# Kernel tuning notes

Hardware: AMD Instinct MI355X
Metric: run time of the kernel (lower is better)

## Reference

```python
import jax, jax.numpy as jnp
import numpy as np

B, D, W, KVAL = 8192, 768, 8192, 32  # batch, input_dim, width, mp_kval


def setup_inputs() -> dict:
    key = jax.random.key(0)
    k1, k2 = jax.random.split(key)
    x = jax.random.normal(k1, (B, D), dtype=jnp.float32)
    # decoder dictionary Ad: [input_dim, width], kaiming-ish scale
    Ad = jax.random.normal(k2, (D, W), dtype=jnp.float32) / np.float32(np.sqrt(D))
    bd = jnp.zeros((1, D), dtype=jnp.float32)
    return {"x": x, "Ad": Ad, "bd": bd}


def reference(x, Ad, bd):
    # Matching-pursuit branch of SAE.forward (sae_type == 'MP')
    Ad_n = Ad / jnp.clip(jnp.linalg.norm(Ad, axis=0, keepdims=True), 1e-8)  # [D, W]
    resid0 = x - bd                                    # [B, D]
    codes0 = jnp.zeros((x.shape[0], Ad.shape[1]), x.dtype)  # [B, W]
    sel0 = jnp.zeros_like(codes0)                      # [B, W]
    rows = jnp.arange(x.shape[0])

    def step(carry, _):
        resid, codes, sel = carry
        z = resid @ Ad_n                               # [B, W] projection
        z = jnp.where(sel > 0, 0.0, z)                 # mask already-selected atoms
        idx = jnp.argmax(jnp.abs(z), axis=1)           # [B] greedy top-1
        val = jnp.take_along_axis(z, idx[:, None], axis=1)  # [B, 1]
        codes = codes.at[rows, idx].add(val[:, 0])
        sel = sel.at[rows, idx].add(1.0)
        # rank-1 residual update: (one_hot(idx)*val) @ Ad_n.T == val * Ad_n[:, idx].T
        resid = resid - val * jnp.take(Ad_n.T, idx, axis=0)  # [B, D]
        return (resid, codes, sel), None

    (resid, codes, sel), _ = jax.lax.scan(step, (resid0, codes0, sel0), None, length=KVAL)
    return codes @ Ad_n.T + bd
```

## Files before the change

### kernel.cpp

```cpp
#include <hip/hip_runtime.h>
#include <cstddef>

static const int WW = 8192;
static const int DD = 768;
static const int BBATCH = 8192;
static const int KSEL = 32;

typedef double f64x4 __attribute__((ext_vector_type(4)));

__device__ inline void mfma_f64_probe(int lane, int* pi, int* pj) {
    f64x4 z0{0.0, 0.0, 0.0, 0.0};
    f64x4 d1 = __builtin_amdgcn_mfma_f64_16x16x4f64((double)lane, 1.0, z0, 0, 0, 0);
    f64x4 d2 = __builtin_amdgcn_mfma_f64_16x16x4f64(1.0, (double)lane, z0, 0, 0, 0);
#pragma unroll
    for (int v = 0; v < 4; ++v) {
        pi[v] = (((int)d1[v] - 96) >> 2) & 15;
        pj[v] = (((int)d2[v] - 96) >> 2) & 15;
    }
}

__global__ __launch_bounds__(256) void colnorm_kernel(const float* __restrict__ Ad,
                                                      float* __restrict__ nrm) {
    int w = blockIdx.x * 256 + threadIdx.x;
    double s = 0.0;
    for (int d = 0; d < DD; ++d) {
        double v = (double)Ad[(size_t)d * WW + w];
        s += v * v;
    }
    nrm[w] = fmaxf((float)sqrt(s), 1e-8f);
}

__global__ __launch_bounds__(256) void transpose_scale_kernel(const float* __restrict__ Ad,
                                                              const float* __restrict__ nrm,
                                                              float* __restrict__ AdnT) {
    __shared__ float tile[32][33];
    int wb = blockIdx.x * 32;
    int db = blockIdx.y * 32;
    int tx = threadIdx.x;
    int ty = threadIdx.y;
    for (int i = ty; i < 32; i += 8)
        tile[i][tx] = Ad[(size_t)(db + i) * WW + (wb + tx)];
    __syncthreads();
    for (int i = ty; i < 32; i += 8)
        AdnT[(size_t)(wb + i) * DD + (db + tx)] = tile[tx][i] / nrm[wb + i];
}

__global__ __launch_bounds__(256, 2) void gram_mfma_f64_kernel(const float* __restrict__ Ad,
                                                               const float* __restrict__ nrm,
                                                               float* __restrict__ G) {
    const int bx = blockIdx.x, by = blockIdx.y;
    if (bx < 2 * by) return;
    __shared__ __align__(16) double As[32 * 130];
    __shared__ __align__(16) double Bs[32 * 66];
    const int tid = threadIdx.x;
    const int lane = tid & 63;
    const int wv = tid >> 6;
    const int wr = wv >> 1;
    const int wc = wv & 1;
    const int i0 = by * 128;
    const int j0 = bx * 64;
    const int ar0 = tid >> 6;
    const int ap0 = (tid & 63) * 2;
    const int brow = tid >> 5;
    const int bpos = (tid & 31) * 2;

    f64x4 acc[4][2];
#pragma unroll
    for (int m = 0; m < 4; ++m)
#pragma unroll
        for (int n = 0; n < 2; ++n)
            acc[m][n] = f64x4{0.0, 0.0, 0.0, 0.0};

    float2 aL[8], bl[4];
#pragma unroll
    for (int q = 0; q < 8; ++q)
        aL[q] = *(const float2*)&Ad[(size_t)(4 * q + ar0) * WW + i0 + ap0];
#pragma unroll
    for (int s = 0; s < 4; ++s)
        bl[s] = *(const float2*)&Ad[(size_t)(8 * s + brow) * WW + j0 + bpos];

    for (int k0 = 0; k0 < DD; k0 += 32) {
        __syncthreads();
#pragma unroll
        for (int q = 0; q < 8; ++q) {
            double2 da; da.x = (double)aL[q].x; da.y = (double)aL[q].y;
            *(double2*)&As[(4 * q + ar0) * 130 + ap0] = da;
        }
#pragma unroll
        for (int s = 0; s < 4; ++s) {
            double2 d0; d0.x = (double)bl[s].x; d0.y = (double)bl[s].y;
            *(double2*)&Bs[(8 * s + brow) * 66 + bpos] = d0;
        }
        __syncthreads();
        if (k0 + 32 < DD) {
#pragma unroll
            for (int q = 0; q < 8; ++q)
                aL[q] = *(const float2*)&Ad[(size_t)(k0 + 32 + 4 * q + ar0) * WW + i0 + ap0];
#pragma unroll
            for (int s = 0; s < 4; ++s)
                bl[s] = *(const float2*)&Ad[(size_t)(k0 + 32 + 8 * s + brow) * WW + j0 + bpos];
        }
#pragma unroll
        for (int kc = 0; kc < 8; ++kc) {
            const int krow = kc * 4 + (lane >> 4);
            const double* ap = &As[krow * 130 + wr * 64 + (lane & 15)];
            const double* bp = &Bs[krow * 66 + wc * 32 + (lane & 15)];
            double aF[4], bF[2];
#pragma unroll
            for (int m = 0; m < 4; ++m) aF[m] = ap[m * 16];
#pragma unroll
            for (int n = 0; n < 2; ++n) bF[n] = bp[n * 16];
#pragma unroll
            for (int m = 0; m < 4; ++m)
#pragma unroll
                for (int n = 0; n < 2; ++n)
                    acc[m][n] = __builtin_amdgcn_mfma_f64_16x16x4f64(aF[m], bF[n],
                                                                     acc[m][n], 0, 0, 0);
        }
    }

    int pi[4], pj[4];
    mfma_f64_probe(lane, pi, pj);
#pragma unroll
    for (int m = 0; m < 4; ++m) {
#pragma unroll
        for (int v = 0; v < 4; ++v) {
            int row = i0 + wr * 64 + m * 16 + pi[v];
            double inv_i = 1.0 / (double)nrm[row];
#pragma unroll
            for (int n = 0; n < 2; ++n) {
                int col = j0 + wc * 32 + n * 16 + pj[v];
                G[(size_t)row * WW + col] = (float)(acc[m][n][v] * inv_i / (double)nrm[col]);
            }
        }
    }
}

__global__ __launch_bounds__(256) void mirror_kernel(float* __restrict__ G) {
    const int ti = blockIdx.y;
    const int tj = blockIdx.x;
    if (tj <= ti) return;
    __shared__ float tile[64][65];
    const int t = threadIdx.x;
    const int c4 = (t & 15) * 4;
    const int r  = t >> 4;
#pragma unroll
    for (int rr = r; rr < 64; rr += 16) {
        float4 v = *(const float4*)&G[(size_t)(ti * 64 + rr) * WW + tj * 64 + c4];
        tile[rr][c4 + 0] = v.x;
        tile[rr][c4 + 1] = v.y;
        tile[rr][c4 + 2] = v.z;
        tile[rr][c4 + 3] = v.w;
    }
    __syncthreads();
#pragma unroll
    for (int rr = r; rr < 64; rr += 16) {
        float4 v = make_float4(tile[c4 + 0][rr], tile[c4 + 1][rr],
                               tile[c4 + 2][rr], tile[c4 + 3][rr]);
        *(float4*)&G[(size_t)(tj * 64 + rr) * WW + ti * 64 + c4] = v;
    }
}

__global__ __launch_bounds__(256, 2) void z_mfma_f64_kernel(const float* __restrict__ X,
                                                            const float* __restrict__ Ad,
                                                            const float* __restrict__ bd,
                                                            const float* __restrict__ nrm,
                                                            float* __restrict__ Z) {
    __shared__ __align__(16) double As[32 * 66];
    __shared__ __align__(16) double Bs[32 * 130];
    const int tid = threadIdx.x;
    const int lane = tid & 63;
    const int wc = tid >> 6;
    const int b0 = blockIdx.y * 64;
    const int w0 = blockIdx.x * 128;
    const int r  = tid >> 2;
    const int k8 = (tid & 3) * 8;
    const int br0 = tid >> 6;
    const int bp0 = (tid & 63) * 2;

    f64x4 acc[4][2];
#pragma unroll
    for (int m = 0; m < 4; ++m)
#pragma unroll
        for (int n = 0; n < 2; ++n)
            acc[m][n] = f64x4{0.0, 0.0, 0.0, 0.0};

    float4 a0L, a1L; float2 bL[8];
    {
        float4 bias0 = *(const float4*)&bd[k8];
        float4 bias1 = *(const float4*)&bd[k8 + 4];
        float4 a0 = *(const float4*)&X[(size_t)(b0 + r) * DD + k8];
        float4 a1 = *(const float4*)&X[(size_t)(b0 + r) * DD + k8 + 4];
        a0.x -= bias0.x; a0.y -= bias0.y; a0.z -= bias0.z; a0.w -= bias0.w;
        a1.x -= bias1.x; a1.y -= bias1.y; a1.z -= bias1.z; a1.w -= bias1.w;
        a0L = a0; a1L = a1;
#pragma unroll
        for (int q = 0; q < 8; ++q)
            bL[q] = *(const float2*)&Ad[(size_t)(4 * q + br0) * WW + w0 + bp0];
    }

    for (int k0 = 0; k0 < DD; k0 += 32) {
        __syncthreads();
        As[(k8 + 0) * 66 + r] = (double)a0L.x;
        As[(k8 + 1) * 66 + r] = (double)a0L.y;
        As[(k8 + 2) * 66 + r] = (double)a0L.z;
        As[(k8 + 3) * 66 + r] = (double)a0L.w;
        As[(k8 + 4) * 66 + r] = (double)a1L.x;
        As[(k8 + 5) * 66 + r] = (double)a1L.y;
        As[(k8 + 6) * 66 + r] = (double)a1L.z;
        As[(k8 + 7) * 66 + r] = (double)a1L.w;
#pragma unroll
        for (int q = 0; q < 8; ++q) {
            double2 db; db.x = (double)bL[q].x; db.y = (double)bL[q].y;
            *(double2*)&Bs[(4 * q + br0) * 130 + bp0] = db;
        }
        __syncthreads();
        if (k0 + 32 < DD) {
            const int kn = k0 + 32;
            float4 bias0 = *(const float4*)&bd[kn + k8];
            float4 bias1 = *(const float4*)&bd[kn + k8 + 4];
            float4 a0 = *(const float4*)&X[(size_t)(b0 + r) * DD + kn + k8];
            float4 a1 = *(const float4*)&X[(size_t)(b0 + r) * DD + kn + k8 + 4];
            a0.x -= bias0.x; a0.y -= bias0.y; a0.z -= bias0.z; a0.w -= bias0.w;
            a1.x -= bias1.x; a1.y -= bias1.y; a1.z -= bias1.z; a1.w -= bias1.w;
            a0L = a0; a1L = a1;
#pragma unroll
            for (int q = 0; q < 8; ++q)
                bL[q] = *(const float2*)&Ad[(size_t)(kn + 4 * q + br0) * WW + w0 + bp0];
        }
#pragma unroll
        for (int kc = 0; kc < 8; ++kc) {
            const int krow = kc * 4 + (lane >> 4);
            const double* ap = &As[krow * 66 + (lane & 15)];
            const double* bp = &Bs[krow * 130 + wc * 32 + (lane & 15)];
            double aF[4], bF[2];
#pragma unroll
            for (int m = 0; m < 4; ++m) aF[m] = ap[m * 16];
#pragma unroll
            for (int n = 0; n < 2; ++n) bF[n] = bp[n * 16];
#pragma unroll
            for (int m = 0; m < 4; ++m)
#pragma unroll
                for (int n = 0; n < 2; ++n)
                    acc[m][n] = __builtin_amdgcn_mfma_f64_16x16x4f64(aF[m], bF[n],
                                                                     acc[m][n], 0, 0, 0);
        }
    }

    int pi[4], pj[4];
    mfma_f64_probe(lane, pi, pj);
#pragma unroll
    for (int m = 0; m < 4; ++m) {
#pragma unroll
        for (int v = 0; v < 4; ++v) {
            int row = b0 + m * 16 + pi[v];
#pragma unroll
            for (int n = 0; n < 2; ++n) {
                int col = w0 + wc * 32 + n * 16 + pj[v];
                Z[(size_t)row * WW + col] = (float)(acc[m][n][v] / (double)nrm[col]);
            }
        }
    }
}

__global__ __launch_bounds__(256) void mp_loop_kernel(const float* __restrict__ z0,
                                                      const float* __restrict__ G,
                                                      int* __restrict__ idxL,
                                                      float* __restrict__ valL) {
    __shared__ __align__(16) float zrow[WW];
    __shared__ float wv[4];
    __shared__ int   wi[4];
    const int b = blockIdx.x;
    const int t = threadIdx.x;
    float4* zs = (float4*)zrow;

    float best = -1.f;
    int bidx = 0;
    unsigned selmask = 0;

    {
        const float4* zp = (const float4*)(z0 + (size_t)b * WW);
#pragma unroll
        for (int j = 0; j < 8; ++j) {
            int slot = t + 256 * j;
            float4 v = zp[slot];
            zs[slot] = v;
            int w = slot * 4;
            float a0 = fabsf(v.x), a1 = fabsf(v.y), a2 = fabsf(v.z), a3 = fabsf(v.w);
            if (a0 > best) { best = a0; bidx = w; }
            if (a1 > best) { best = a1; bidx = w + 1; }
            if (a2 > best) { best = a2; bidx = w + 2; }
            if (a3 > best) { best = a3; bidx = w + 3; }
        }
    }

    for (int k = 0; k < KSEL; ++k) {
        float v = best;
        int i = bidx;
#pragma unroll
        for (int off = 32; off > 0; off >>= 1) {
            float ov = __shfl_xor(v, off, 64);
            int   oi = __shfl_xor(i, off, 64);
            if (ov > v || (ov == v && oi < i)) { v = ov; i = oi; }
        }
        if ((t & 63) == 0) { wv[t >> 6] = v; wi[t >> 6] = i; }
        __syncthreads();
        float rv = wv[0];
        int   ri = wi[0];
#pragma unroll
        for (int q = 1; q < 4; ++q) {
            float qv = wv[q];
            int   qi = wi[q];
            if (qv > rv || (qv == rv && qi < ri)) { rv = qv; ri = qi; }
        }
        const int idx = ri;
        const float val = zrow[idx];
        if (t == 0) {
            idxL[(size_t)b * KSEL + k] = idx;
            valL[(size_t)b * KSEL + k] = val;
        }
        if (((idx >> 2) & 255) == t)
            selmask |= 1u << (((idx >> 10) << 2) | (idx & 3));
        if (k == KSEL - 1) break;
        __syncthreads();

        best = -1.f;
        bidx = 0;
        const float4* gr = (const float4*)(G + (size_t)idx * WW);
#pragma unroll
        for (int j = 0; j < 8; ++j) {
            int slot = t + 256 * j;
            float4 g = gr[slot];
            float4 z = zs[slot];
            unsigned m = (selmask >> (j * 4)) & 0xFu;
            float n0 = (m & 1u) ? 0.f : z.x - val * g.x;
            float n1 = (m & 2u) ? 0.f : z.y - val * g.y;
            float n2 = (m & 4u) ? 0.f : z.z - val * g.z;
            float n3 = (m & 8u) ? 0.f : z.w - val * g.w;
            zs[slot] = make_float4(n0, n1, n2, n3);
            int w = slot * 4;
            float a0 = fabsf(n0), a1 = fabsf(n1), a2 = fabsf(n2), a3 = fabsf(n3);
            if (a0 > best) { best = a0; bidx = w; }
            if (a1 > best) { best = a1; bidx = w + 1; }
            if (a2 > best) { best = a2; bidx = w + 2; }
            if (a3 > best) { best = a3; bidx = w + 3; }
        }
    }
}

__global__ __launch_bounds__(256) void copy_meta_kernel(const int* __restrict__ si,
                                                        const float* __restrict__ sv,
                                                        int* __restrict__ di,
                                                        float* __restrict__ dv,
                                                        int n) {
    int i = blockIdx.x * 256 + threadIdx.x;
    if (i < n) {
        di[i] = si[i];
        dv[i] = sv[i];
    }
}

__global__ __launch_bounds__(256) void assemble_kernel(const float* __restrict__ AdnT,
                                                       const float* __restrict__ bd,
                                                       const int* __restrict__ idxL,
                                                       const float* __restrict__ valL,
                                                       float* __restrict__ out,
                                                       int rowStart) {
    __shared__ int sidx[KSEL];
    __shared__ float sval[KSEL];
    const int b = blockIdx.x;
    const int row = rowStart + b;
    const int t = threadIdx.x;
    if (t < KSEL) {
        sidx[t] = idxL[(size_t)b * KSEL + t];
        sval[t] = valL[(size_t)b * KSEL + t];
    }
    __syncthreads();
    float acc0 = bd[t];
    float acc1 = bd[t + 256];
    float acc2 = bd[t + 512];
#pragma unroll 4
    for (int k = 0; k < KSEL; ++k) {
        const float* col = AdnT + (size_t)sidx[k] * DD;
        float v = sval[k];
        acc0 += v * col[t];
        acc1 += v * col[t + 256];
        acc2 += v * col[t + 512];
    }
    out[(size_t)row * DD + t] = acc0;
    out[(size_t)row * DD + t + 256] = acc1;
    out[(size_t)row * DD + t + 512] = acc2;
}

extern "C" void kernel_launch(void* const* d_in, const int* in_sizes, int n_in,
                              void* d_out, int out_size, void* d_ws, size_t ws_size,
                              hipStream_t stream) {
    const float* x  = (const float*)d_in[0];
    const float* Ad = (const float*)d_in[1];
    const float* bd = (const float*)d_in[2];
    float* out = (float*)d_out;

    const size_t ADNT_B = (size_t)WW * DD * 4;
    const size_t NRM_B  = (size_t)WW * 4;
    const size_t IDX_B  = (size_t)BBATCH * KSEL * 4;
    const size_t VAL_B  = IDX_B;
    const size_t G_B    = (size_t)WW * WW * 4;
    const size_t ZROW_B = (size_t)WW * 4;
    const size_t A_MIN  = ADNT_B + NRM_B + IDX_B + VAL_B + G_B + 128 * ZROW_B;

    if (ws_size >= A_MIN) {
        char* p = (char*)d_ws;
        float* AdnT = (float*)p;  p += ADNT_B;
        float* nrm  = (float*)p;  p += NRM_B;
        int*   idxL = (int*)p;    p += IDX_B;
        float* valL = (float*)p;  p += VAL_B;
        float* G    = (float*)p;  p += G_B;
        float* z    = (float*)p;
        size_t z_avail = ws_size - (ADNT_B + NRM_B + IDX_B + VAL_B + G_B);
        int chunk = (int)((z_avail / ZROW_B) / 128) * 128;
        if (chunk > BBATCH) chunk = BBATCH;

        colnorm_kernel<<<WW / 256, 256, 0, stream>>>(Ad, nrm);
        gram_mfma_f64_kernel<<<dim3(WW / 64, WW / 128), 256, 0, stream>>>(Ad, nrm, G);
        mirror_kernel<<<dim3(WW / 64, WW / 64), 256, 0, stream>>>(G);
        for (int r0 = 0; r0 < BBATCH; r0 += chunk) {
            int rows = (BBATCH - r0 < chunk) ? (BBATCH - r0) : chunk;
            z_mfma_f64_kernel<<<dim3(WW / 128, rows / 64), 256, 0, stream>>>(
                x + (size_t)r0 * DD, Ad, bd, nrm, z);
            mp_loop_kernel<<<rows, 256, 0, stream>>>(
                z, G, idxL + (size_t)r0 * KSEL, valL + (size_t)r0 * KSEL);
        }
        transpose_scale_kernel<<<dim3(WW / 32, DD / 32), dim3(32, 8), 0, stream>>>(Ad, nrm, AdnT);
        assemble_kernel<<<BBATCH, 256, 0, stream>>>(AdnT, bd, idxL, valL, out, 0);
    } else if (ws_size >= G_B) {
        float* G    = (float*)d_ws;
        char*  ob   = (char*)d_out;
        float* z    = (float*)ob;
        float* nrm  = (float*)(ob + 20971520);
        int*   idxL = (int*)(ob + 23068672);
        float* valL = (float*)(ob + 24117248);
        float* AdnT = (float*)d_ws;
        int*   idx2 = (int*)((char*)d_ws + ADNT_B);
        float* val2 = (float*)((char*)d_ws + ADNT_B + IDX_B);
        const int chunk = 512;

        colnorm_kernel<<<WW / 256, 256, 0, stream>>>(Ad, nrm);
        gram_mfma_f64_kernel<<<dim3(WW / 64, WW / 128), 256, 0, stream>>>(Ad, nrm, G);
        mirror_kernel<<<dim3(WW / 64, WW / 64), 256, 0, stream>>>(G);
        for (int r0 = 0; r0 < BBATCH; r0 += chunk) {
            int rows = (BBATCH - r0 < chunk) ? (BBATCH - r0) : chunk;
            z_mfma_f64_kernel<<<dim3(WW / 128, rows / 64), 256, 0, stream>>>(
                x + (size_t)r0 * DD, Ad, bd, nrm, z);
            mp_loop_kernel<<<rows, 256, 0, stream>>>(
                z, G, idxL + (size_t)r0 * KSEL, valL + (size_t)r0 * KSEL);
        }
        {
            int n = BBATCH * KSEL;
            copy_meta_kernel<<<(n + 255) / 256, 256, 0, stream>>>(idxL, valL, idx2, val2, n);
        }
        transpose_scale_kernel<<<dim3(WW / 32, DD / 32), dim3(32, 8), 0, stream>>>(Ad, nrm, AdnT);
        assemble_kernel<<<BBATCH, 256, 0, stream>>>(AdnT, bd, idx2, val2, out, 0);
    }
}
```

Baseline: 4.459 ms.

## Fuse z-projection and MP loop into one pipelined kernel with double-buffered chunks

Replaces the alternating z_mfma and mp_loop launches with one fused kernel per step. In each launch, some blocks run the matching-pursuit loop on chunk i-1 while other blocks compute the z projection for chunk i into the other half of a double buffer, so the compute-bound GEMM overlaps the latency-bound MP loop. Chunk size drops to 256 rows. Separately, the Gram kernel's K-tile shrinks from 32 to 16 to cut shared memory per block. The cost is more launches and heterogeneous blocks sharing a 49KB shared-memory footprint, which may limit occupancy.

```diff
diff --git a/kernel.cpp b/kernel.cpp
--- a/kernel.cpp
+++ b/kernel.cpp
@@ -50,8 +50,8 @@
                                                                float* __restrict__ G) {
     const int bx = blockIdx.x, by = blockIdx.y;
     if (bx < 2 * by) return;
-    __shared__ __align__(16) double As[32 * 130];
-    __shared__ __align__(16) double Bs[32 * 66];
+    __shared__ __align__(16) double As[16 * 130];
+    __shared__ __align__(16) double Bs[16 * 66];
     const int tid = threadIdx.x;
     const int lane = tid & 63;
     const int wv = tid >> 6;
@@ -71,37 +71,36 @@
         for (int n = 0; n < 2; ++n)
             acc[m][n] = f64x4{0.0, 0.0, 0.0, 0.0};
 
-    float2 aL[8], bl[4];
-#pragma unroll
-    for (int q = 0; q < 8; ++q)
+    float2 aL[4], bl0, bl1;
+#pragma unroll
+    for (int q = 0; q < 4; ++q)
         aL[q] = *(const float2*)&Ad[(size_t)(4 * q + ar0) * WW + i0 + ap0];
-#pragma unroll
-    for (int s = 0; s < 4; ++s)
-        bl[s] = *(const float2*)&Ad[(size_t)(8 * s + brow) * WW + j0 + bpos];
-
-    for (int k0 = 0; k0 < DD; k0 += 32) {
-        __syncthreads();
-#pragma unroll
-        for (int q = 0; q < 8; ++q) {
+    bl0 = *(const float2*)&Ad[(size_t)(brow) * WW + j0 + bpos];
+    bl1 = *(const float2*)&Ad[(size_t)(8 + brow) * WW + j0 + bpos];
+
+    for (int k0 = 0; k0 < DD; k0 += 16) {
+        __syncthreads();
+#pragma unroll
+        for (int q = 0; q < 4; ++q) {
             double2 da; da.x = (double)aL[q].x; da.y = (double)aL[q].y;
             *(double2*)&As[(4 * q + ar0) * 130 + ap0] = da;
         }
-#pragma unroll
-        for (int s = 0; s < 4; ++s) {
-            double2 d0; d0.x = (double)bl[s].x; d0.y = (double)bl[s].y;
-            *(double2*)&Bs[(8 * s + brow) * 66 + bpos] = d0;
-        }
-        __syncthreads();
-        if (k0 + 32 < DD) {
-#pragma unroll
-            for (int q = 0; q < 8; ++q)
-                aL[q] = *(const float2*)&Ad[(size_t)(k0 + 32 + 4 * q + ar0) * WW + i0 + ap0];
-#pragma unroll
-            for (int s = 0; s < 4; ++s)
-                bl[s] = *(const float2*)&Ad[(size_t)(k0 + 32 + 8 * s + brow) * WW + j0 + bpos];
-        }
-#pragma unroll
-        for (int kc = 0; kc < 8; ++kc) {
+        {
+            double2 d0; d0.x = (double)bl0.x; d0.y = (double)bl0.y;
+            double2 d1; d1.x = (double)bl1.x; d1.y = (double)bl1.y;
+            *(double2*)&Bs[brow * 66 + bpos] = d0;
+            *(double2*)&Bs[(8 + brow) * 66 + bpos] = d1;
+        }
+        __syncthreads();
+        if (k0 + 16 < DD) {
+#pragma unroll
+            for (int q = 0; q < 4; ++q)
+                aL[q] = *(const float2*)&Ad[(size_t)(k0 + 16 + 4 * q + ar0) * WW + i0 + ap0];
+            bl0 = *(const float2*)&Ad[(size_t)(k0 + 16 + brow) * WW + j0 + bpos];
+            bl1 = *(const float2*)&Ad[(size_t)(k0 + 24 + brow) * WW + j0 + bpos];
+        }
+#pragma unroll
+        for (int kc = 0; kc < 4; ++kc) {
             const int krow = kc * 4 + (lane >> 4);
             const double* ap = &As[krow * 130 + wr * 64 + (lane & 15)];
             const double* bp = &Bs[krow * 66 + wc * 32 + (lane & 15)];
@@ -161,18 +160,20 @@
     }
 }
 
-__global__ __launch_bounds__(256, 2) void z_mfma_f64_kernel(const float* __restrict__ X,
-                                                            const float* __restrict__ Ad,
-                                                            const float* __restrict__ bd,
-                                                            const float* __restrict__ nrm,
-                                                            float* __restrict__ Z) {
-    __shared__ __align__(16) double As[32 * 66];
-    __shared__ __align__(16) double Bs[32 * 130];
+__device__ __forceinline__ void z_body(char* smem,
+                                       const float* __restrict__ X,
+                                       const float* __restrict__ Ad,
+                                       const float* __restrict__ bd,
+                                       const float* __restrict__ nrm,
+                                       float* __restrict__ Z,
+                                       int bx, int by) {
+    double* As = (double*)smem;
+    double* Bs = (double*)(smem + 16896);
     const int tid = threadIdx.x;
     const int lane = tid & 63;
-    const int wc = tid >> 6;
-    const int b0 = blockIdx.y * 64;
-    const int w0 = blockIdx.x * 128;
+    const int wcol = tid >> 6;
+    const int b0 = by * 64;
+    const int w0 = bx * 128;
     const int r  = tid >> 2;
     const int k8 = (tid & 3) * 8;
     const int br0 = tid >> 6;
@@ -232,7 +233,7 @@
         for (int kc = 0; kc < 8; ++kc) {
             const int krow = kc * 4 + (lane >> 4);
             const double* ap = &As[krow * 66 + (lane & 15)];
-            const double* bp = &Bs[krow * 130 + wc * 32 + (lane & 15)];
+            const double* bp = &Bs[krow * 130 + wcol * 32 + (lane & 15)];
             double aF[4], bF[2];
 #pragma unroll
             for (int m = 0; m < 4; ++m) aF[m] = ap[m * 16];
@@ -256,21 +257,22 @@
             int row = b0 + m * 16 + pi[v];
 #pragma unroll
             for (int n = 0; n < 2; ++n) {
-                int col = w0 + wc * 32 + n * 16 + pj[v];
+                int col = w0 + wcol * 32 + n * 16 + pj[v];
                 Z[(size_t)row * WW + col] = (float)(acc[m][n][v] / (double)nrm[col]);
             }
         }
     }
 }
 
-__global__ __launch_bounds__(256) void mp_loop_kernel(const float* __restrict__ z0,
-                                                      const float* __restrict__ G,
-                                                      int* __restrict__ idxL,
-                                                      float* __restrict__ valL) {
-    __shared__ __align__(16) float zrow[WW];
-    __shared__ float wv[4];
-    __shared__ int   wi[4];
-    const int b = blockIdx.x;
+__device__ __forceinline__ void mp_body(char* smem,
+                                        const float* __restrict__ z0,
+                                        const float* __restrict__ G,
+                                        int* __restrict__ idxL,
+                                        float* __restrict__ valL,
+                                        int b) {
+    float* zrow = (float*)smem;
+    float* wv   = (float*)(smem + 32768);
+    int*   wi   = (int*)(smem + 32784);
     const int t = threadIdx.x;
     float4* zs = (float4*)zrow;
 
@@ -348,6 +350,26 @@
     }
 }
 
+__global__ __launch_bounds__(256, 2) void zmp_fused_kernel(const float* __restrict__ X,
+                                                           const float* __restrict__ Ad,
+                                                           const float* __restrict__ bd,
+                                                           const float* __restrict__ nrm,
+                                                           const float* __restrict__ G,
+                                                           float* __restrict__ zOut,
+                                                           const float* __restrict__ zIn,
+                                                           int* __restrict__ idxL,
+                                                           float* __restrict__ valL,
+                                                           int mpBlocks) {
+    __shared__ __align__(16) char smem[50176];
+    const int id = blockIdx.x;
+    if (id < mpBlocks) {
+        mp_body(smem, zIn, G, idxL, valL, id);
+    } else {
+        const int zid = id - mpBlocks;
+        z_body(smem, X, Ad, bd, nrm, zOut, zid & 63, zid >> 6);
+    }
+}
+
 __global__ __launch_bounds__(256) void copy_meta_kernel(const int* __restrict__ si,
                                                         const float* __restrict__ sv,
                                                         int* __restrict__ di,
@@ -392,6 +414,24 @@
     out[(size_t)row * DD + t + 512] = acc2;
 }
 
+static void run_zmp_pipeline(const float* x, const float* Ad, const float* bd,
+                             const float* nrm, const float* G,
+                             float* zbuf0, float* zbuf1, int CH,
+                             int* idxL, float* valL, hipStream_t stream) {
+    const int nCh = BBATCH / CH;
+    for (int i = 0; i <= nCh; ++i) {
+        const int zr  = (i < nCh) ? CH : 0;
+        const int mpr = (i > 0) ? CH : 0;
+        const int zb  = 64 * (zr / 64);
+        float* zout = (i & 1) ? zbuf1 : zbuf0;
+        const float* zin = (i & 1) ? zbuf0 : zbuf1;
+        int*   idxP = (i > 0) ? idxL + (size_t)(i - 1) * CH * KSEL : idxL;
+        float* valP = (i > 0) ? valL + (size_t)(i - 1) * CH * KSEL : valL;
+        zmp_fused_kernel<<<mpr + zb, 256, 0, stream>>>(
+            x + (size_t)i * CH * DD, Ad, bd, nrm, G, zout, zin, idxP, valP, mpr);
+    }
+}
+
 extern "C" void kernel_launch(void* const* d_in, const int* in_sizes, int n_in,
                               void* d_out, int out_size, void* d_ws, size_t ws_size,
                               hipStream_t stream) {
@@ -417,43 +457,33 @@
         float* G    = (float*)p;  p += G_B;
         float* z    = (float*)p;
         size_t z_avail = ws_size - (ADNT_B + NRM_B + IDX_B + VAL_B + G_B);
-        int chunk = (int)((z_avail / ZROW_B) / 128) * 128;
-        if (chunk > BBATCH) chunk = BBATCH;
+        int CH = 256;
+        while (CH > 64 && (size_t)2 * CH * ZROW_B > z_avail) CH >>= 1;
+        float* zbuf0 = z;
+        float* zbuf1 = z + (size_t)CH * WW;
 
         colnorm_kernel<<<WW / 256, 256, 0, stream>>>(Ad, nrm);
         gram_mfma_f64_kernel<<<dim3(WW / 64, WW / 128), 256, 0, stream>>>(Ad, nrm, G);
         mirror_kernel<<<dim3(WW / 64, WW / 64), 256, 0, stream>>>(G);
-        for (int r0 = 0; r0 < BBATCH; r0 += chunk) {
-            int rows = (BBATCH - r0 < chunk) ? (BBATCH - r0) : chunk;
-            z_mfma_f64_kernel<<<dim3(WW / 128, rows / 64), 256, 0, stream>>>(
-                x + (size_t)r0 * DD, Ad, bd, nrm, z);
-            mp_loop_kernel<<<rows, 256, 0, stream>>>(
-                z, G, idxL + (size_t)r0 * KSEL, valL + (size_t)r0 * KSEL);
-        }
+        run_zmp_pipeline(x, Ad, bd, nrm, G, zbuf0, zbuf1, CH, idxL, valL, stream);
         transpose_scale_kernel<<<dim3(WW / 32, DD / 32), dim3(32, 8), 0, stream>>>(Ad, nrm, AdnT);
         assemble_kernel<<<BBATCH, 256, 0, stream>>>(AdnT, bd, idxL, valL, out, 0);
     } else if (ws_size >= G_B) {
         float* G    = (float*)d_ws;
         char*  ob   = (char*)d_out;
-        float* z    = (float*)ob;
+        float* zbuf0 = (float*)ob;
+        float* zbuf1 = (float*)(ob + (size_t)256 * ZROW_B);
         float* nrm  = (float*)(ob + 20971520);
         int*   idxL = (int*)(ob + 23068672);
         float* valL = (float*)(ob + 24117248);
         float* AdnT = (float*)d_ws;
         int*   idx2 = (int*)((char*)d_ws + ADNT_B);
         float* val2 = (float*)((char*)d_ws + ADNT_B + IDX_B);
-        const int chunk = 512;
 
         colnorm_kernel<<<WW / 256, 256, 0, stream>>>(Ad, nrm);
         gram_mfma_f64_kernel<<<dim3(WW / 64, WW / 128), 256, 0, stream>>>(Ad, nrm, G);
         mirror_kernel<<<dim3(WW / 64, WW / 64), 256, 0, stream>>>(G);
-        for (int r0 = 0; r0 < BBATCH; r0 += chunk) {
-            int rows = (BBATCH - r0 < chunk) ? (BBATCH - r0) : chunk;
-            z_mfma_f64_kernel<<<dim3(WW / 128, rows / 64), 256, 0, stream>>>(
-                x + (size_t)r0 * DD, Ad, bd, nrm, z);
-            mp_loop_kernel<<<rows, 256, 0, stream>>>(
-                z, G, idxL + (size_t)r0 * KSEL, valL + (size_t)r0 * KSEL);
-        }
+        run_zmp_pipeline(x, Ad, bd, nrm, G, zbuf0, zbuf1, 256, idxL, valL, stream);
         {
             int n = BBATCH * KSEL;
             copy_meta_kernel<<<(n + 255) / 256, 256, 0, stream>>>(idxL, valL, idx2, val2, n);
```

After: 4.841 ms. 8.6% more time.

## Process two batch rows per block in MP loop and shrink Gram k-tile

Applied to the files above, without the earlier changes.

The matching-pursuit loop kernel now handles two batch rows per block. Each block keeps two residual-projection rows in shared memory and interleaves their reductions and Gram-row updates. This adds memory-level parallelism and halves the number of barriers per row, at the cost of 64KB of shared memory per block, which may lower occupancy. Separately, the Gram kernel's k-tile drops from 32 to 16, halving its LDS footprint and prefetch registers so more blocks can stay resident, in exchange for twice as many sync iterations.

```diff
diff --git a/kernel.cpp b/kernel.cpp
--- a/kernel.cpp
+++ b/kernel.cpp
@@ -50,8 +50,8 @@
                                                                float* __restrict__ G) {
     const int bx = blockIdx.x, by = blockIdx.y;
     if (bx < 2 * by) return;
-    __shared__ __align__(16) double As[32 * 130];
-    __shared__ __align__(16) double Bs[32 * 66];
+    __shared__ __align__(16) double As[16 * 130];
+    __shared__ __align__(16) double Bs[16 * 66];
     const int tid = threadIdx.x;
     const int lane = tid & 63;
     const int wv = tid >> 6;
@@ -71,37 +71,36 @@
         for (int n = 0; n < 2; ++n)
             acc[m][n] = f64x4{0.0, 0.0, 0.0, 0.0};
 
-    float2 aL[8], bl[4];
-#pragma unroll
-    for (int q = 0; q < 8; ++q)
+    float2 aL[4], bl0, bl1;
+#pragma unroll
+    for (int q = 0; q < 4; ++q)
         aL[q] = *(const float2*)&Ad[(size_t)(4 * q + ar0) * WW + i0 + ap0];
-#pragma unroll
-    for (int s = 0; s < 4; ++s)
-        bl[s] = *(const float2*)&Ad[(size_t)(8 * s + brow) * WW + j0 + bpos];
-
-    for (int k0 = 0; k0 < DD; k0 += 32) {
-        __syncthreads();
-#pragma unroll
-        for (int q = 0; q < 8; ++q) {
+    bl0 = *(const float2*)&Ad[(size_t)(brow) * WW + j0 + bpos];
+    bl1 = *(const float2*)&Ad[(size_t)(8 + brow) * WW + j0 + bpos];
+
+    for (int k0 = 0; k0 < DD; k0 += 16) {
+        __syncthreads();
+#pragma unroll
+        for (int q = 0; q < 4; ++q) {
             double2 da; da.x = (double)aL[q].x; da.y = (double)aL[q].y;
             *(double2*)&As[(4 * q + ar0) * 130 + ap0] = da;
         }
-#pragma unroll
-        for (int s = 0; s < 4; ++s) {
-            double2 d0; d0.x = (double)bl[s].x; d0.y = (double)bl[s].y;
-            *(double2*)&Bs[(8 * s + brow) * 66 + bpos] = d0;
-        }
-        __syncthreads();
-        if (k0 + 32 < DD) {
-#pragma unroll
-            for (int q = 0; q < 8; ++q)
-                aL[q] = *(const float2*)&Ad[(size_t)(k0 + 32 + 4 * q + ar0) * WW + i0 + ap0];
-#pragma unroll
-            for (int s = 0; s < 4; ++s)
-                bl[s] = *(const float2*)&Ad[(size_t)(k0 + 32 + 8 * s + brow) * WW + j0 + bpos];
-        }
-#pragma unroll
-        for (int kc = 0; kc < 8; ++kc) {
+        {
+            double2 d0; d0.x = (double)bl0.x; d0.y = (double)bl0.y;
+            double2 d1; d1.x = (double)bl1.x; d1.y = (double)bl1.y;
+            *(double2*)&Bs[brow * 66 + bpos] = d0;
+            *(double2*)&Bs[(8 + brow) * 66 + bpos] = d1;
+        }
+        __syncthreads();
+        if (k0 + 16 < DD) {
+#pragma unroll
+            for (int q = 0; q < 4; ++q)
+                aL[q] = *(const float2*)&Ad[(size_t)(k0 + 16 + 4 * q + ar0) * WW + i0 + ap0];
+            bl0 = *(const float2*)&Ad[(size_t)(k0 + 16 + brow) * WW + j0 + bpos];
+            bl1 = *(const float2*)&Ad[(size_t)(k0 + 24 + brow) * WW + j0 + bpos];
+        }
+#pragma unroll
+        for (int kc = 0; kc < 4; ++kc) {
             const int krow = kc * 4 + (lane >> 4);
             const double* ap = &As[krow * 130 + wr * 64 + (lane & 15)];
             const double* bp = &Bs[krow * 66 + wc * 32 + (lane & 15)];
@@ -170,7 +169,7 @@
     __shared__ __align__(16) double Bs[32 * 130];
     const int tid = threadIdx.x;
     const int lane = tid & 63;
-    const int wc = tid >> 6;
+    const int wcol = tid >> 6;
     const int b0 = blockIdx.y * 64;
     const int w0 = blockIdx.x * 128;
     const int r  = tid >> 2;
@@ -232,7 +231,7 @@
         for (int kc = 0; kc < 8; ++kc) {
             const int krow = kc * 4 + (lane >> 4);
             const double* ap = &As[krow * 66 + (lane & 15)];
-            const double* bp = &Bs[krow * 130 + wc * 32 + (lane & 15)];
+            const double* bp = &Bs[krow * 130 + wcol * 32 + (lane & 15)];
             double aF[4], bF[2];
 #pragma unroll
             for (int m = 0; m < 4; ++m) aF[m] = ap[m * 16];
@@ -256,94 +255,130 @@
             int row = b0 + m * 16 + pi[v];
 #pragma unroll
             for (int n = 0; n < 2; ++n) {
-                int col = w0 + wc * 32 + n * 16 + pj[v];
+                int col = w0 + wcol * 32 + n * 16 + pj[v];
                 Z[(size_t)row * WW + col] = (float)(acc[m][n][v] / (double)nrm[col]);
             }
         }
     }
 }
 
-__global__ __launch_bounds__(256) void mp_loop_kernel(const float* __restrict__ z0,
-                                                      const float* __restrict__ G,
-                                                      int* __restrict__ idxL,
-                                                      float* __restrict__ valL) {
-    __shared__ __align__(16) float zrow[WW];
-    __shared__ float wv[4];
-    __shared__ int   wi[4];
-    const int b = blockIdx.x;
+__global__ __launch_bounds__(256) void mp_loop2_kernel(const float* __restrict__ z0,
+                                                       const float* __restrict__ G,
+                                                       int* __restrict__ idxL,
+                                                       float* __restrict__ valL) {
+    __shared__ __align__(16) float zrow0[WW];
+    __shared__ __align__(16) float zrow1[WW];
+    __shared__ float wv0[4], wv1[4];
+    __shared__ int   wi0[4], wi1[4];
+    const int b0 = blockIdx.x * 2;
     const int t = threadIdx.x;
-    float4* zs = (float4*)zrow;
-
-    float best = -1.f;
-    int bidx = 0;
-    unsigned selmask = 0;
+    float4* zs0 = (float4*)zrow0;
+    float4* zs1 = (float4*)zrow1;
+
+    float best0 = -1.f, best1 = -1.f;
+    int bi0 = 0, bi1 = 0;
+    unsigned sm0 = 0, sm1 = 0;
 
     {
-        const float4* zp = (const float4*)(z0 + (size_t)b * WW);
+        const float4* zp0 = (const float4*)(z0 + (size_t)b0 * WW);
+        const float4* zp1 = (const float4*)(z0 + (size_t)(b0 + 1) * WW);
 #pragma unroll
         for (int j = 0; j < 8; ++j) {
             int slot = t + 256 * j;
-            float4 v = zp[slot];
-            zs[slot] = v;
+            float4 v0 = zp0[slot];
+            float4 v1 = zp1[slot];
+            zs0[slot] = v0;
+            zs1[slot] = v1;
             int w = slot * 4;
-            float a0 = fabsf(v.x), a1 = fabsf(v.y), a2 = fabsf(v.z), a3 = fabsf(v.w);
-            if (a0 > best) { best = a0; bidx = w; }
-            if (a1 > best) { best = a1; bidx = w + 1; }
-            if (a2 > best) { best = a2; bidx = w + 2; }
-            if (a3 > best) { best = a3; bidx = w + 3; }
+            float a0 = fabsf(v0.x), a1 = fabsf(v0.y), a2 = fabsf(v0.z), a3 = fabsf(v0.w);
+            if (a0 > best0) { best0 = a0; bi0 = w; }
+            if (a1 > best0) { best0 = a1; bi0 = w + 1; }
+            if (a2 > best0) { best0 = a2; bi0 = w + 2; }
+            if (a3 > best0) { best0 = a3; bi0 = w + 3; }
+            float c0 = fabsf(v1.x), c1 = fabsf(v1.y), c2 = fabsf(v1.z), c3 = fabsf(v1.w);
+            if (c0 > best1) { best1 = c0; bi1 = w; }
+            if (c1 > best1) { best1 = c1; bi1 = w + 1; }
+            if (c2 > best1) { best1 = c2; bi1 = w + 2; }
+            if (c3 > best1) { best1 = c3; bi1 = w + 3; }
         }
     }
 
     for (int k = 0; k < KSEL; ++k) {
-        float v = best;
-        int i = bidx;
+        float v0 = best0, v1 = best1;
+        int i0 = bi0, i1 = bi1;
 #pragma unroll
         for (int off = 32; off > 0; off >>= 1) {
-            float ov = __shfl_xor(v, off, 64);
-            int   oi = __shfl_xor(i, off, 64);
-            if (ov > v || (ov == v && oi < i)) { v = ov; i = oi; }
-        }
-        if ((t & 63) == 0) { wv[t >> 6] = v; wi[t >> 6] = i; }
-        __syncthreads();
-        float rv = wv[0];
-        int   ri = wi[0];
+            float ov0 = __shfl_xor(v0, off, 64);
+            int   oi0 = __shfl_xor(i0, off, 64);
+            float ov1 = __shfl_xor(v1, off, 64);
+            int   oi1 = __shfl_xor(i1, off, 64);
+            if (ov0 > v0 || (ov0 == v0 && oi0 < i0)) { v0 = ov0; i0 = oi0; }
+            if (ov1 > v1 || (ov1 == v1 && oi1 < i1)) { v1 = ov1; i1 = oi1; }
+        }
+        if ((t & 63) == 0) {
+            wv0[t >> 6] = v0; wi0[t >> 6] = i0;
+            wv1[t >> 6] = v1; wi1[t >> 6] = i1;
+        }
+        __syncthreads();
+        float rv0 = wv0[0], rv1 = wv1[0];
+        int   ri0 = wi0[0], ri1 = wi1[0];
 #pragma unroll
         for (int q = 1; q < 4; ++q) {
-            float qv = wv[q];
-            int   qi = wi[q];
-            if (qv > rv || (qv == rv && qi < ri)) { rv = qv; ri = qi; }
-        }
-        const int idx = ri;
-        const float val = zrow[idx];
+            float q0 = wv0[q], q1 = wv1[q];
+            int   j0 = wi0[q], j1 = wi1[q];
+            if (q0 > rv0 || (q0 == rv0 && j0 < ri0)) { rv0 = q0; ri0 = j0; }
+            if (q1 > rv1 || (q1 == rv1 && j1 < ri1)) { rv1 = q1; ri1 = j1; }
+        }
+        const int idx0 = ri0, idx1 = ri1;
+        const float val0 = zrow0[idx0];
+        const float val1 = zrow1[idx1];
         if (t == 0) {
-            idxL[(size_t)b * KSEL + k] = idx;
-            valL[(size_t)b * KSEL + k] = val;
-        }
-        if (((idx >> 2) & 255) == t)
-            selmask |= 1u << (((idx >> 10) << 2) | (idx & 3));
+            idxL[(size_t)b0 * KSEL + k] = idx0;
+            valL[(size_t)b0 * KSEL + k] = val0;
+            idxL[(size_t)(b0 + 1) * KSEL + k] = idx1;
+            valL[(size_t)(b0 + 1) * KSEL + k] = val1;
+        }
+        if (((idx0 >> 2) & 255) == t)
+            sm0 |= 1u << (((idx0 >> 10) << 2) | (idx0 & 3));
+        if (((idx1 >> 2) & 255) == t)
+            sm1 |= 1u << (((idx1 >> 10) << 2) | (idx1 & 3));
         if (k == KSEL - 1) break;
         __syncthreads();
 
-        best = -1.f;
-        bidx = 0;
-        const float4* gr = (const float4*)(G + (size_t)idx * WW);
+        best0 = -1.f; bi0 = 0;
+        best1 = -1.f; bi1 = 0;
+        const float4* gr0 = (const float4*)(G + (size_t)idx0 * WW);
+        const float4* gr1 = (const float4*)(G + (size_t)idx1 * WW);
 #pragma unroll
         for (int j = 0; j < 8; ++j) {
             int slot = t + 256 * j;
-            float4 g = gr[slot];
-            float4 z = zs[slot];
-            unsigned m = (selmask >> (j * 4)) & 0xFu;
-            float n0 = (m & 1u) ? 0.f : z.x - val * g.x;
-            float n1 = (m & 2u) ? 0.f : z.y - val * g.y;
-            float n2 = (m & 4u) ? 0.f : z.z - val * g.z;
-            float n3 = (m & 8u) ? 0.f : z.w - val * g.w;
-            zs[slot] = make_float4(n0, n1, n2, n3);
+            float4 g0 = gr0[slot];
+            float4 g1 = gr1[slot];
+            float4 z0v = zs0[slot];
+            float4 z1v = zs1[slot];
+            unsigned m0 = (sm0 >> (j * 4)) & 0xFu;
+            unsigned m1 = (sm1 >> (j * 4)) & 0xFu;
+            float n00 = (m0 & 1u) ? 0.f : z0v.x - val0 * g0.x;
+            float n01 = (m0 & 2u) ? 0.f : z0v.y - val0 * g0.y;
+            float n02 = (m0 & 4u) ? 0.f : z0v.z - val0 * g0.z;
+            float n03 = (m0 & 8u) ? 0.f : z0v.w - val0 * g0.w;
+            float n10 = (m1 & 1u) ? 0.f : z1v.x - val1 * g1.x;
+            float n11 = (m1 & 2u) ? 0.f : z1v.y - val1 * g1.y;
+            float n12 = (m1 & 4u) ? 0.f : z1v.z - val1 * g1.z;
+            float n13 = (m1 & 8u) ? 0.f : z1v.w - val1 * g1.w;
+            zs0[slot] = make_float4(n00, n01, n02, n03);
+            zs1[slot] = make_float4(n10, n11, n12, n13);
             int w = slot * 4;
-            float a0 = fabsf(n0), a1 = fabsf(n1), a2 = fabsf(n2), a3 = fabsf(n3);
-            if (a0 > best) { best = a0; bidx = w; }
-            if (a1 > best) { best = a1; bidx = w + 1; }
-            if (a2 > best) { best = a2; bidx = w + 2; }
-            if (a3 > best) { best = a3; bidx = w + 3; }
+            float a0 = fabsf(n00), a1 = fabsf(n01), a2 = fabsf(n02), a3 = fabsf(n03);
+            if (a0 > best0) { best0 = a0; bi0 = w; }
+            if (a1 > best0) { best0 = a1; bi0 = w + 1; }
+            if (a2 > best0) { best0 = a2; bi0 = w + 2; }
+            if (a3 > best0) { best0 = a3; bi0 = w + 3; }
+            float c0 = fabsf(n10), c1 = fabsf(n11), c2 = fabsf(n12), c3 = fabsf(n13);
+            if (c0 > best1) { best1 = c0; bi1 = w; }
+            if (c1 > best1) { best1 = c1; bi1 = w + 1; }
+            if (c2 > best1) { best1 = c2; bi1 = w + 2; }
+            if (c3 > best1) { best1 = c3; bi1 = w + 3; }
         }
     }
 }
@@ -427,7 +462,7 @@
             int rows = (BBATCH - r0 < chunk) ? (BBATCH - r0) : chunk;
             z_mfma_f64_kernel<<<dim3(WW / 128, rows / 64), 256, 0, stream>>>(
                 x + (size_t)r0 * DD, Ad, bd, nrm, z);
-            mp_loop_kernel<<<rows, 256, 0, stream>>>(
+            mp_loop2_kernel<<<rows / 2, 256, 0, stream>>>(
                 z, G, idxL + (size_t)r0 * KSEL, valL + (size_t)r0 * KSEL);
         }
         transpose_scale_kernel<<<dim3(WW / 32, DD / 32), dim3(32, 8), 0, stream>>>(Ad, nrm, AdnT);
@@ -451,7 +486,7 @@
             int rows = (BBATCH - r0 < chunk) ? (BBATCH - r0) : chunk;
             z_mfma_f64_kernel<<<dim3(WW / 128, rows / 64), 256, 0, stream>>>(
                 x + (size_t)r0 * DD, Ad, bd, nrm, z);
-            mp_loop_kernel<<<rows, 256, 0, stream>>>(
+            mp_loop2_kernel<<<rows / 2, 256, 0, stream>>>(
                 z, G, idxL + (size_t)r0 * KSEL, valL + (size_t)r0 * KSEL);
         }
         {
```

New measurement: 5.337 ms. 1.2x slower.

## Keep MP residual row in registers and shrink Gram kernel K-tile

Applied to the files above, without the earlier changes.

The matching-pursuit loop kernel now holds each thread's 32 projection values in registers instead of a 32 KB shared-memory row. The selected value is taken from the owning thread and broadcast through one shared scalar. This frees most of the per-block LDS, so more blocks can be resident. The Gram MFMA kernel halves its K-tile from 32 to 16 to cut its LDS footprint, at the cost of twice as many barrier and staging rounds. The fallback path's batch chunk rises from 512 to 640 rows, giving fewer z/mp launch pairs.

```diff
diff --git a/kernel.cpp b/kernel.cpp
--- a/kernel.cpp
+++ b/kernel.cpp
@@ -50,8 +50,8 @@
                                                                float* __restrict__ G) {
     const int bx = blockIdx.x, by = blockIdx.y;
     if (bx < 2 * by) return;
-    __shared__ __align__(16) double As[32 * 130];
-    __shared__ __align__(16) double Bs[32 * 66];
+    __shared__ __align__(16) double As[16 * 130];
+    __shared__ __align__(16) double Bs[16 * 66];
     const int tid = threadIdx.x;
     const int lane = tid & 63;
     const int wv = tid >> 6;
@@ -71,37 +71,36 @@
         for (int n = 0; n < 2; ++n)
             acc[m][n] = f64x4{0.0, 0.0, 0.0, 0.0};
 
-    float2 aL[8], bl[4];
-#pragma unroll
-    for (int q = 0; q < 8; ++q)
+    float2 aL[4], bl0, bl1;
+#pragma unroll
+    for (int q = 0; q < 4; ++q)
         aL[q] = *(const float2*)&Ad[(size_t)(4 * q + ar0) * WW + i0 + ap0];
-#pragma unroll
-    for (int s = 0; s < 4; ++s)
-        bl[s] = *(const float2*)&Ad[(size_t)(8 * s + brow) * WW + j0 + bpos];
-
-    for (int k0 = 0; k0 < DD; k0 += 32) {
-        __syncthreads();
-#pragma unroll
-        for (int q = 0; q < 8; ++q) {
+    bl0 = *(const float2*)&Ad[(size_t)(brow) * WW + j0 + bpos];
+    bl1 = *(const float2*)&Ad[(size_t)(8 + brow) * WW + j0 + bpos];
+
+    for (int k0 = 0; k0 < DD; k0 += 16) {
+        __syncthreads();
+#pragma unroll
+        for (int q = 0; q < 4; ++q) {
             double2 da; da.x = (double)aL[q].x; da.y = (double)aL[q].y;
             *(double2*)&As[(4 * q + ar0) * 130 + ap0] = da;
         }
-#pragma unroll
-        for (int s = 0; s < 4; ++s) {
-            double2 d0; d0.x = (double)bl[s].x; d0.y = (double)bl[s].y;
-            *(double2*)&Bs[(8 * s + brow) * 66 + bpos] = d0;
-        }
-        __syncthreads();
-        if (k0 + 32 < DD) {
-#pragma unroll
-            for (int q = 0; q < 8; ++q)
-                aL[q] = *(const float2*)&Ad[(size_t)(k0 + 32 + 4 * q + ar0) * WW + i0 + ap0];
-#pragma unroll
-            for (int s = 0; s < 4; ++s)
-                bl[s] = *(const float2*)&Ad[(size_t)(k0 + 32 + 8 * s + brow) * WW + j0 + bpos];
-        }
-#pragma unroll
-        for (int kc = 0; kc < 8; ++kc) {
+        {
+            double2 d0; d0.x = (double)bl0.x; d0.y = (double)bl0.y;
+            double2 d1; d1.x = (double)bl1.x; d1.y = (double)bl1.y;
+            *(double2*)&Bs[brow * 66 + bpos] = d0;
+            *(double2*)&Bs[(8 + brow) * 66 + bpos] = d1;
+        }
+        __syncthreads();
+        if (k0 + 16 < DD) {
+#pragma unroll
+            for (int q = 0; q < 4; ++q)
+                aL[q] = *(const float2*)&Ad[(size_t)(k0 + 16 + 4 * q + ar0) * WW + i0 + ap0];
+            bl0 = *(const float2*)&Ad[(size_t)(k0 + 16 + brow) * WW + j0 + bpos];
+            bl1 = *(const float2*)&Ad[(size_t)(k0 + 24 + brow) * WW + j0 + bpos];
+        }
+#pragma unroll
+        for (int kc = 0; kc < 4; ++kc) {
             const int krow = kc * 4 + (lane >> 4);
             const double* ap = &As[krow * 130 + wr * 64 + (lane & 15)];
             const double* bp = &Bs[krow * 66 + wc * 32 + (lane & 15)];
@@ -170,7 +169,7 @@
     __shared__ __align__(16) double Bs[32 * 130];
     const int tid = threadIdx.x;
     const int lane = tid & 63;
-    const int wc = tid >> 6;
+    const int wcol = tid >> 6;
     const int b0 = blockIdx.y * 64;
     const int w0 = blockIdx.x * 128;
     const int r  = tid >> 2;
@@ -232,7 +231,7 @@
         for (int kc = 0; kc < 8; ++kc) {
             const int krow = kc * 4 + (lane >> 4);
             const double* ap = &As[krow * 66 + (lane & 15)];
-            const double* bp = &Bs[krow * 130 + wc * 32 + (lane & 15)];
+            const double* bp = &Bs[krow * 130 + wcol * 32 + (lane & 15)];
             double aF[4], bF[2];
 #pragma unroll
             for (int m = 0; m < 4; ++m) aF[m] = ap[m * 16];
@@ -256,24 +255,24 @@
             int row = b0 + m * 16 + pi[v];
 #pragma unroll
             for (int n = 0; n < 2; ++n) {
-                int col = w0 + wc * 32 + n * 16 + pj[v];
+                int col = w0 + wcol * 32 + n * 16 + pj[v];
                 Z[(size_t)row * WW + col] = (float)(acc[m][n][v] / (double)nrm[col]);
             }
         }
     }
 }
 
-__global__ __launch_bounds__(256) void mp_loop_kernel(const float* __restrict__ z0,
-                                                      const float* __restrict__ G,
-                                                      int* __restrict__ idxL,
-                                                      float* __restrict__ valL) {
-    __shared__ __align__(16) float zrow[WW];
+__global__ __launch_bounds__(256) void mp_loop_reg_kernel(const float* __restrict__ z0,
+                                                          const float* __restrict__ G,
+                                                          int* __restrict__ idxL,
+                                                          float* __restrict__ valL) {
     __shared__ float wv[4];
     __shared__ int   wi[4];
+    __shared__ float sval;
     const int b = blockIdx.x;
     const int t = threadIdx.x;
-    float4* zs = (float4*)zrow;
-
+
+    float4 zr[8];
     float best = -1.f;
     int bidx = 0;
     unsigned selmask = 0;
@@ -284,7 +283,7 @@
         for (int j = 0; j < 8; ++j) {
             int slot = t + 256 * j;
             float4 v = zp[slot];
-            zs[slot] = v;
+            zr[j] = v;
             int w = slot * 4;
             float a0 = fabsf(v.x), a1 = fabsf(v.y), a2 = fabsf(v.z), a3 = fabsf(v.w);
             if (a0 > best) { best = a0; bidx = w; }
@@ -314,15 +313,26 @@
             if (qv > rv || (qv == rv && qi < ri)) { rv = qv; ri = qi; }
         }
         const int idx = ri;
-        const float val = zrow[idx];
+        if (((idx >> 2) & 255) == t) {
+            float myv = 0.f;
+#pragma unroll
+            for (int j = 0; j < 8; ++j) {
+                if ((idx >> 10) == j) {
+                    float4 q = zr[j];
+                    int e = idx & 3;
+                    myv = (e == 0) ? q.x : (e == 1) ? q.y : (e == 2) ? q.z : q.w;
+                }
+            }
+            sval = myv;
+            selmask |= 1u << (((idx >> 10) << 2) | (idx & 3));
+        }
+        __syncthreads();
+        const float val = sval;
         if (t == 0) {
             idxL[(size_t)b * KSEL + k] = idx;
             valL[(size_t)b * KSEL + k] = val;
         }
-        if (((idx >> 2) & 255) == t)
-            selmask |= 1u << (((idx >> 10) << 2) | (idx & 3));
         if (k == KSEL - 1) break;
-        __syncthreads();
 
         best = -1.f;
         bidx = 0;
@@ -331,13 +341,13 @@
         for (int j = 0; j < 8; ++j) {
             int slot = t + 256 * j;
             float4 g = gr[slot];
-            float4 z = zs[slot];
+            float4 z = zr[j];
             unsigned m = (selmask >> (j * 4)) & 0xFu;
             float n0 = (m & 1u) ? 0.f : z.x - val * g.x;
             float n1 = (m & 2u) ? 0.f : z.y - val * g.y;
             float n2 = (m & 4u) ? 0.f : z.z - val * g.z;
             float n3 = (m & 8u) ? 0.f : z.w - val * g.w;
-            zs[slot] = make_float4(n0, n1, n2, n3);
+            zr[j] = make_float4(n0, n1, n2, n3);
             int w = slot * 4;
             float a0 = fabsf(n0), a1 = fabsf(n1), a2 = fabsf(n2), a3 = fabsf(n3);
             if (a0 > best) { best = a0; bidx = w; }
@@ -427,7 +437,7 @@
             int rows = (BBATCH - r0 < chunk) ? (BBATCH - r0) : chunk;
             z_mfma_f64_kernel<<<dim3(WW / 128, rows / 64), 256, 0, stream>>>(
                 x + (size_t)r0 * DD, Ad, bd, nrm, z);
-            mp_loop_kernel<<<rows, 256, 0, stream>>>(
+            mp_loop_reg_kernel<<<rows, 256, 0, stream>>>(
                 z, G, idxL + (size_t)r0 * KSEL, valL + (size_t)r0 * KSEL);
         }
         transpose_scale_kernel<<<dim3(WW / 32, DD / 32), dim3(32, 8), 0, stream>>>(Ad, nrm, AdnT);
@@ -442,7 +452,7 @@
         float* AdnT = (float*)d_ws;
         int*   idx2 = (int*)((char*)d_ws + ADNT_B);
         float* val2 = (float*)((char*)d_ws + ADNT_B + IDX_B);
-        const int chunk = 512;
+        const int chunk = 640;
 
         colnorm_kernel<<<WW / 256, 256, 0, stream>>>(Ad, nrm);
         gram_mfma_f64_kernel<<<dim3(WW / 64, WW / 128), 256, 0, stream>>>(Ad, nrm, G);
@@ -451,7 +461,7 @@
             int rows = (BBATCH - r0 < chunk) ? (BBATCH - r0) : chunk;
             z_mfma_f64_kernel<<<dim3(WW / 128, rows / 64), 256, 0, stream>>>(
                 x + (size_t)r0 * DD, Ad, bd, nrm, z);
-            mp_loop_kernel<<<rows, 256, 0, stream>>>(
+            mp_loop_reg_kernel<<<rows, 256, 0, stream>>>(
                 z, G, idxL + (size_t)r0 * KSEL, valL + (size_t)r0 * KSEL);
         }
         {
```

After: 4.781 ms. 7.2% more time.
